# Performance work log

Hardware: AMD Instinct MI355X
Metric: run time of the kernel (lower is better)

The kernel has to match this reference:

```python
import jax, jax.numpy as jnp
import numpy as np

B, C, H, W, L = 8, 512, 32, 32, 10
CQK = C // 8
EPS = 1e-5


def conv1x1(x, Wt, b):
    # 1x1 conv == per-pixel linear: [O,C] x [B,C,H,W] -> [B,O,H,W]
    return jnp.einsum('oc,bchw->bohw', Wt, x) + b[None, :, None, None]


def batchnorm_train(x, g, b):
    # BatchNorm2d in training mode: batch stats over (N,H,W), biased variance
    m = x.mean(axis=(0, 2, 3))
    v = x.var(axis=(0, 2, 3))
    inv = jax.lax.rsqrt(v + EPS)
    return (x - m[None, :, None, None]) * (g * inv)[None, :, None, None] + b[None, :, None, None]


def setup_inputs() -> dict:
    key = jax.random.key(0)
    ks = jax.random.split(key, 24)
    s = lambda n: 1.0 / np.sqrt(n)
    inp = {
        'x': jax.random.normal(ks[0], (B, C, H, W), jnp.float32),
        'y': jax.random.normal(ks[1], (B, C, H, W), jnp.float32),
        'x_hidden': jax.random.normal(ks[2], (L, B, C, H, W), jnp.float32),
        'y_hidden': jax.random.normal(ks[3], (L, B, C, H, W), jnp.float32),
        'qW': jax.random.normal(ks[4], (CQK, C), jnp.float32) * s(C),
        'qb': jnp.zeros((CQK,), jnp.float32),
        'kW': jax.random.normal(ks[5], (CQK, C), jnp.float32) * s(C),
        'kb': jnp.zeros((CQK,), jnp.float32),
        'v1W': jax.random.normal(ks[6], (C, C), jnp.float32) * s(C),
        'v1b': jnp.zeros((C,), jnp.float32),
        'v2W': jax.random.normal(ks[7], (C, C), jnp.float32) * s(C),
        'v2b': jnp.zeros((C,), jnp.float32),
        'hw1': jnp.ones((L,), jnp.float32),
        'hw2': jnp.ones((L,), jnp.float32),
        'g1W1': jax.random.normal(ks[8], (64, C), jnp.float32) * s(C),
        'g1b1': jnp.zeros((64,), jnp.float32),
        'g1W2': jax.random.normal(ks[9], (1, 64), jnp.float32) * s(64),
        'g1b2': jnp.zeros((1,), jnp.float32),
        'g2W1': jax.random.normal(ks[10], (64, C), jnp.float32) * s(C),
        'g2b1': jnp.zeros((64,), jnp.float32),
        'g2W2': jax.random.normal(ks[11], (1, 64), jnp.float32) * s(64),
        'g2b2': jnp.zeros((1,), jnp.float32),
        'rW1': jax.random.normal(ks[12], (C, C), jnp.float32) * s(C),
        'rb1': jnp.zeros((C,), jnp.float32),
        'bn1g': jnp.ones((C,), jnp.float32),
        'bn1b': jnp.zeros((C,), jnp.float32),
        'rW2': jax.random.normal(ks[13], (C, C), jnp.float32) * s(C),
        'rb2': jnp.zeros((C,), jnp.float32),
        'bn2g': jnp.ones((C,), jnp.float32),
        'bn2b': jnp.zeros((C,), jnp.float32),
    }
    return inp


def reference(x, y, x_hidden, y_hidden, qW, qb, kW, kb, v1W, v1b, v2W, v2b,
              hw1, hw2, g1W1, g1b1, g1W2, g1b2, g2W1, g2b1, g2W2, g2b2,
              rW1, rb1, bn1g, bn1b, rW2, rb2, bn2g, bn2b):
    b_, c_, h_, w_ = x.shape
    n = h_ * w_

    def residual(z):
        z1 = jax.nn.relu(batchnorm_train(conv1x1(z, rW1, rb1), bn1g, bn1b))
        return batchnorm_train(conv1x1(z1, rW2, rb2), bn2g, bn2b)

    # QKV projections (1x1 convs), flattened to tokens
    q = conv1x1(x, qW, qb).reshape(b_, CQK, n).transpose(0, 2, 1)   # [B,N,Cqk]
    k = conv1x1(y, kW, kb).reshape(b_, CQK, n)                       # [B,Cqk,N]
    v1 = conv1x1(x, v1W, v1b).reshape(b_, c_, n)                     # [B,C,N]
    v2 = conv1x1(y, v2W, v2b).reshape(b_, c_, n)

    attn = jax.nn.softmax(jnp.einsum('bnd,bdm->bnm', q, k), axis=-1)  # [B,N,N]
    out1 = jnp.einsum('bcn,bmn->bcm', v1, attn).reshape(b_, c_, h_, w_)  # v1 @ attn^T
    out2 = jnp.einsum('bcn,bnm->bcm', v2, attn).reshape(b_, c_, h_, w_)  # v2 @ attn

    # hidden-layer weighted channel means -> gamma scalars
    num_layers = min(x_hidden.shape[0], L)
    xw = jax.nn.softmax(hw1[:num_layers])
    yw = jax.nn.softmax(hw2[:num_layers])
    x_hw = jnp.einsum('l,lbc->bc', xw, x_hidden[:num_layers].mean(axis=(3, 4)))  # [B,C]
    y_hw = jnp.einsum('l,lbc->bc', yw, y_hidden[:num_layers].mean(axis=(3, 4)))

    def gamma_gen(v, W1, b1, W2, b2):
        h1 = jax.nn.relu(v @ W1.T + b1)
        return (h1 @ W2.T + b2).reshape(b_, 1, 1, 1)

    gamma1 = gamma_gen(x_hw, g1W1, g1b1, g1W2, g1b2)
    gamma2 = gamma_gen(y_hw, g2W1, g2b1, g2W2, g2b2)

    out1 = jax.nn.relu(residual(gamma1 * out1) + x)
    out2 = jax.nn.relu(residual(gamma2 * out2) + y)
    return out1, out2
```

## Files before the change

kernel.cpp:

```cpp
#include <hip/hip_runtime.h>

#define BB 8
#define CC 512
#define NT 1024
#define LL 10
#define DQK 64
#define BN_EPS 1e-5f

using u16 = unsigned short;
typedef __attribute__((ext_vector_type(8))) short short8;
typedef __attribute__((ext_vector_type(4))) float f32x4;
typedef __attribute__((ext_vector_type(4))) float nf4;

__device__ __forceinline__ float waveSum(float v) {
#pragma unroll
  for (int o = 32; o; o >>= 1) v += __shfl_down(v, o, 64);
  return v;
}
__device__ __forceinline__ float waveMax(float v) {
#pragma unroll
  for (int o = 32; o; o >>= 1) v = fmaxf(v, __shfl_down(v, o, 64));
  return v;
}
__device__ __forceinline__ u16 f2bf(float f) {
  unsigned u = __float_as_uint(f);
  u += 0x7FFFu + ((u >> 16) & 1u);
  return (u16)(u >> 16);
}
__device__ __forceinline__ float bf2f(u16 h) {
  return __uint_as_float(((unsigned)h) << 16);
}
__device__ __forceinline__ void g2l16(const u16* g, void* l) {
  __builtin_amdgcn_global_load_lds(
      (const __attribute__((address_space(1))) unsigned int*)g,
      (__attribute__((address_space(3))) unsigned int*)l, 16, 0, 0);
}

struct PreArgs {
  const float *xh, *yh;
  float* lm;
  const float *v1W, *v2W, *rW1, *rW2;
  u16* Wdst;
  const float *qW, *kW;
  u16 *qh, *ql, *kh, *kl;
  const float *qb, *kb, *v1b, *v2b;
  float *qkb, *vb;
  const float *x, *y;
  u16 *xth, *xtl, *yth, *ytl;
};
__global__ __launch_bounds__(256) void pre_kernel(PreArgs a) {
  __shared__ float t[64][65];
  const int blk = blockIdx.x;
  if (blk < 20480) {
    int wid = blk * 4 + (threadIdx.x >> 6);
    int lane = threadIdx.x & 63;
    const int LBC = LL * BB * CC;
    const float* src = a.xh;
    int r = wid;
    if (wid >= LBC) { src = a.yh; r = wid - LBC; }
    const nf4* p = (const nf4*)(src + (size_t)r * NT);
    nf4 v0 = __builtin_nontemporal_load(p + lane);
    nf4 v1 = __builtin_nontemporal_load(p + 64 + lane);
    nf4 v2 = __builtin_nontemporal_load(p + 128 + lane);
    nf4 v3 = __builtin_nontemporal_load(p + 192 + lane);
    float s = ((v0.x + v0.y) + (v0.z + v0.w)) + ((v1.x + v1.y) + (v1.z + v1.w)) +
              ((v2.x + v2.y) + (v2.z + v2.w)) + ((v3.x + v3.y) + (v3.z + v3.w));
    s = waveSum(s);
    if (lane == 0) a.lm[wid] = s * (1.0f / NT);
  } else if (blk < 21504) {
    int rel = blk - 20480;
    const float* srcs[4] = {a.v1W, a.v2W, a.rW1, a.rW2};
    const float4* s4 = (const float4*)srcs[rel >> 8];
    int r = rel & 255;
    float4 v = s4[(size_t)r * 256 + threadIdx.x];
    uint2 o;
    o.x = (unsigned)f2bf(v.x) | ((unsigned)f2bf(v.y) << 16);
    o.y = (unsigned)f2bf(v.z) | ((unsigned)f2bf(v.w) << 16);
    ((uint2*)a.Wdst)[(size_t)rel * 256 + threadIdx.x] = o;
  } else if (blk < 21568) {
    int rel = blk - 21504;
    if (rel == 0) {
      int tt = threadIdx.x;
      if (tt < 64) a.qkb[tt] = a.qb[tt];
      else if (tt < 128) a.qkb[tt] = a.kb[tt - 64];
      a.vb[tt] = a.v1b[tt]; a.vb[tt + 256] = a.v1b[tt + 256];
      a.vb[tt + 512] = a.v2b[tt]; a.vb[tt + 768] = a.v2b[tt + 256];
    }
    const float* src = (rel < 32) ? a.qW : a.kW;
    u16* dh = (rel < 32) ? a.qh : a.kh;
    u16* dl = (rel < 32) ? a.ql : a.kl;
    int r = rel & 31;
    float4 v = ((const float4*)src)[(size_t)r * 256 + threadIdx.x];
    u16 h0 = f2bf(v.x), h1 = f2bf(v.y), h2 = f2bf(v.z), h3 = f2bf(v.w);
    u16 l0 = f2bf(v.x - bf2f(h0)), l1 = f2bf(v.y - bf2f(h1));
    u16 l2 = f2bf(v.z - bf2f(h2)), l3 = f2bf(v.w - bf2f(h3));
    uint2 oh, ol;
    oh.x = (unsigned)h0 | ((unsigned)h1 << 16); oh.y = (unsigned)h2 | ((unsigned)h3 << 16);
    ol.x = (unsigned)l0 | ((unsigned)l1 << 16); ol.y = (unsigned)l2 | ((unsigned)l3 << 16);
    ((uint2*)dh)[(size_t)r * 256 + threadIdx.x] = oh;
    ((uint2*)dl)[(size_t)r * 256 + threadIdx.x] = ol;
  } else {
    int rel = blk - 21568;
    int z = rel >> 7;
    const float* src = (z < 8) ? a.x : a.y;
    u16* dh = (z < 8) ? a.xth : a.yth;
    u16* dl = (z < 8) ? a.xtl : a.ytl;
    int b = z & 7;
    int n0 = (rel & 15) * 64, c0 = ((rel >> 4) & 7) * 64;
    int tc = threadIdx.x & 63, tr = threadIdx.x >> 6;
    const float* S = src + ((size_t)b * CC + c0) * NT + n0;
#pragma unroll
    for (int r = 0; r < 16; r++) {
      int c = tr + r * 4;
      t[c][tc] = S[(size_t)c * NT + tc];
    }
    __syncthreads();
    size_t base = ((size_t)b * NT + n0) * CC + c0;
#pragma unroll
    for (int r = 0; r < 16; r++) {
      int n = tr + r * 4;
      float v = t[tc][n];
      u16 h = f2bf(v);
      dh[base + (size_t)n * CC + tc] = h;
      dl[base + (size_t)n * CC + tc] = f2bf(v - bf2f(h));
    }
  }
}

__global__ __launch_bounds__(256) void gamma_kernel(
    const float* __restrict__ lm,
    const float* __restrict__ hw1, const float* __restrict__ hw2,
    const float* __restrict__ g1W1, const float* __restrict__ g1b1,
    const float* __restrict__ g1W2, const float* __restrict__ g1b2,
    const float* __restrict__ g2W1, const float* __restrict__ g2b1,
    const float* __restrict__ g2W2, const float* __restrict__ g2b2,
    float* __restrict__ gamma) {
  int which = blockIdx.x >> 3;
  int b = blockIdx.x & 7;
  const float* hw = which ? hw2 : hw1;
  const float* W1 = which ? g2W1 : g1W1;
  const float* b1 = which ? g2b1 : g1b1;
  const float* W2 = which ? g2W2 : g1W2;
  const float* b2 = which ? g2b2 : g1b2;
  __shared__ float sxhw[CC];
  __shared__ float wsm[LL];
  if (threadIdx.x == 0) {
    float mx = -1e30f;
    for (int l = 0; l < LL; l++) mx = fmaxf(mx, hw[l]);
    float den = 0.f, e[LL];
    for (int l = 0; l < LL; l++) { e[l] = __expf(hw[l] - mx); den += e[l]; }
    for (int l = 0; l < LL; l++) wsm[l] = e[l] / den;
  }
  __syncthreads();
  const float* lmb = lm + (size_t)which * LL * BB * CC + b * CC;
  for (int c = threadIdx.x; c < CC; c += blockDim.x) {
    float a = 0.f;
    for (int l = 0; l < LL; l++) a += wsm[l] * lmb[l * BB * CC + c];
    sxhw[c] = a;
  }
  __syncthreads();
  float contrib = 0.f;
  if (threadIdx.x < 64) {
    int d = threadIdx.x;
    float a = b1[d];
    const float* wr = W1 + d * CC;
    for (int c = 0; c < CC; c++) a = fmaf(wr[c], sxhw[c], a);
    contrib = W2[d] * fmaxf(a, 0.f);
  }
  contrib = waveSum(contrib);
  if (threadIdx.x == 0) gamma[which * BB + b] = contrib + b2[0];
}

__global__ __launch_bounds__(256) void transpose_attn_kernel(
    const u16* __restrict__ attn, u16* __restrict__ attnT) {
  __shared__ u16 t[64][66];
  int b = blockIdx.z;
  int n0 = blockIdx.y * 64, m0 = blockIdx.x * 64;
  int tc = threadIdx.x & 63, tr = threadIdx.x >> 6;
  const u16* S = attn + ((size_t)b * NT + n0) * NT + m0;
#pragma unroll
  for (int r = 0; r < 16; r++) {
    int nr = tr + r * 4;
    t[nr][tc] = S[(size_t)nr * NT + tc];
  }
  __syncthreads();
  u16* D = attnT + ((size_t)b * NT + m0) * NT + n0;
#pragma unroll
  for (int r = 0; r < 16; r++) {
    int mr = tr + r * 4;
    D[(size_t)mr * NT + tc] = t[tc][mr];
  }
}

template <int BN, int SMODE>
__global__ __launch_bounds__(256) void gemm_bf16(
    const u16* __restrict__ A, long long sA, int lda,
    const u16* __restrict__ B, long long sB, long long sB2, int ldb,
    void* __restrict__ C, long long sC, int ldc,
    int K, int storef32,
    const float* __restrict__ bias_row, int brs,
    const float* __restrict__ scale,
    float* __restrict__ pS, float* __restrict__ pS2) {
  constexpr int BM = 128, BK = 32;
  constexpr int WN = (BN == 128) ? 2 : 1;
  constexpr int WM = 4 / WN;
  constexpr int FM = BM / (WM * 16);
  constexpr int FN = BN / (WN * 16);
  __shared__ u16 As[BM * BK];
  __shared__ u16 Bs[BN * BK];
  const int bz = blockIdx.z;
  const int i0 = blockIdx.y * BM;
  const int j0 = blockIdx.x * BN;
  const u16* Ab = A + (size_t)bz * sA + (size_t)i0 * lda;
  const u16* Bb = B + (size_t)(bz & 7) * sB + (size_t)(bz >> 3) * sB2 + (size_t)j0 * ldb;
  const int tid = threadIdx.x;
  const int lane = tid & 63;
  const int wave = tid >> 6;
  const int wr = wave / WN, wc = wave % WN;
  const int fr = lane & 15;
  const int kg = lane >> 4;
  const int arow = tid >> 2;
  const int aq = tid & 3;

  f32x4 acc[FM][FN] = {};

  for (int k0 = 0; k0 < K; k0 += BK) {
#pragma unroll
    for (int c = 0; c < (BM * BK * 2) / 4096; c++)
      g2l16(Ab + (size_t)(arow + c * 64) * lda + k0 + aq * 8,
            (char*)As + c * 4096 + tid * 16);
#pragma unroll
    for (int c = 0; c < (BN * BK * 2) / 4096; c++)
      g2l16(Bb + (size_t)(arow + c * 64) * ldb + k0 + aq * 8,
            (char*)Bs + c * 4096 + tid * 16);
    __syncthreads();
    short8 fa[FM], fb[FN];
#pragma unroll
    for (int i = 0; i < FM; i++)
      fa[i] = *(const short8*)&As[(wr * FM * 16 + i * 16 + fr) * BK + kg * 8];
#pragma unroll
    for (int j = 0; j < FN; j++)
      fb[j] = *(const short8*)&Bs[(wc * FN * 16 + j * 16 + fr) * BK + kg * 8];
#pragma unroll
    for (int i = 0; i < FM; i++)
#pragma unroll
      for (int j = 0; j < FN; j++)
        acc[i][j] = __builtin_amdgcn_mfma_f32_16x16x32_bf16(fa[i], fb[j], acc[i][j], 0, 0, 0);
    __syncthreads();
  }

  const float scl = scale ? scale[bz] : 1.0f;
  const float* brow = bias_row ? bias_row + (size_t)bz * brs : nullptr;
  float* Cf = (float*)C + (size_t)bz * sC;
  u16* Ch = (u16*)C + (size_t)bz * sC;
  float cs[FN] = {}, cs2[FN] = {};
  float rs[FM * 4] = {}, rs2[FM * 4] = {};
#pragma unroll
  for (int i = 0; i < FM; i++) {
#pragma unroll
    for (int j = 0; j < FN; j++) {
      int col = j0 + wc * FN * 16 + j * 16 + fr;
#pragma unroll
      for (int r = 0; r < 4; r++) {
        int row = i0 + wr * FM * 16 + i * 16 + kg * 4 + r;
        float rb = brow ? brow[row] : 0.0f;
        float v = (acc[i][j][r] + rb) * scl;
        if constexpr (SMODE == 1) { cs[j] += v; cs2[j] += v * v; }
        if constexpr (SMODE == 2) { rs[i * 4 + r] += v; rs2[i * 4 + r] += v * v; }
        if (storef32) Cf[(size_t)row * ldc + col] = v;
        else Ch[(size_t)row * ldc + col] = f2bf(v);
      }
    }
  }

  if constexpr (SMODE == 1) {
    __shared__ float sred[2][4][FN][16];
#pragma unroll
    for (int j = 0; j < FN; j++) {
      float s = cs[j], s2 = cs2[j];
      s += __shfl_xor(s, 16, 64); s += __shfl_xor(s, 32, 64);
      s2 += __shfl_xor(s2, 16, 64); s2 += __shfl_xor(s2, 32, 64);
      if (lane < 16) { sred[0][wr][j][lane] = s; sred[1][wr][j][lane] = s2; }
    }
    __syncthreads();
    if (tid < FN * 16) {
      int j = tid >> 4, f = tid & 15;
      float s = sred[0][0][j][f] + sred[0][1][j][f] + sred[0][2][j][f] + sred[0][3][j][f];
      float s2 = sred[1][0][j][f] + sred[1][1][j][f] + sred[1][2][j][f] + sred[1][3][j][f];
      int col = j0 + j * 16 + f;
      int chain = (int)(blockIdx.y >> 6), ib = (int)(blockIdx.y & 63);
      pS[((size_t)chain * 512 + col) * 64 + ib] = s;
      pS2[((size_t)chain * 512 + col) * 64 + ib] = s2;
    }
  }
  if constexpr (SMODE == 2) {
#pragma unroll
    for (int i = 0; i < FM; i++)
#pragma unroll
      for (int r = 0; r < 4; r++) {
        float s = rs[i * 4 + r], s2 = rs2[i * 4 + r];
        s += __shfl_xor(s, 1, 64); s += __shfl_xor(s, 2, 64);
        s += __shfl_xor(s, 4, 64); s += __shfl_xor(s, 8, 64);
        s2 += __shfl_xor(s2, 1, 64); s2 += __shfl_xor(s2, 2, 64);
        s2 += __shfl_xor(s2, 4, 64); s2 += __shfl_xor(s2, 8, 64);
        if (fr == 0) {
          int row = i0 + wr * FM * 16 + i * 16 + kg * 4 + r;
          pS[((size_t)bz * 512 + row) * 128 + blockIdx.x] = s;
          pS2[((size_t)bz * 512 + row) * 128 + blockIdx.x] = s2;
        }
      }
  }
}

__global__ __launch_bounds__(256) void gemm_split(
    const u16* __restrict__ Ah_, const u16* __restrict__ Al_, long long sA, int lda,
    const u16* __restrict__ Bh_, const u16* __restrict__ Bl_, long long sB, int ldb,
    float* __restrict__ Cf, u16* __restrict__ Ch, u16* __restrict__ Cl,
    long long sC, int ldc, int K, const float* __restrict__ bias_col, int bcs) {
  constexpr int BM = 128, BN = 64, BK = 32;
  constexpr int FM = 2, FN = 4;
  __shared__ u16 Ahs[BM * BK];
  __shared__ u16 Als[BM * BK];
  __shared__ u16 Bhs[BN * BK];
  __shared__ u16 Bls[BN * BK];
  const int bz = blockIdx.z;
  const int i0 = blockIdx.y * BM;
  const int j0 = blockIdx.x * BN;
  const u16* Abh = Ah_ + (size_t)bz * sA + (size_t)i0 * lda;
  const u16* Abl = Al_ + (size_t)bz * sA + (size_t)i0 * lda;
  const u16* Bbh = Bh_ + (size_t)bz * sB + (size_t)j0 * ldb;
  const u16* Bbl = Bl_ + (size_t)bz * sB + (size_t)j0 * ldb;
  const int tid = threadIdx.x;
  const int lane = tid & 63;
  const int wr = tid >> 6;
  const int fr = lane & 15;
  const int kg = lane >> 4;
  const int arow = tid >> 2;
  const int aq = tid & 3;

  f32x4 acc[FM][FN] = {};

  for (int k0 = 0; k0 < K; k0 += BK) {
#pragma unroll
    for (int c = 0; c < 2; c++) {
      g2l16(Abh + (size_t)(arow + c * 64) * lda + k0 + aq * 8,
            (char*)Ahs + c * 4096 + tid * 16);
      g2l16(Abl + (size_t)(arow + c * 64) * lda + k0 + aq * 8,
            (char*)Als + c * 4096 + tid * 16);
    }
    g2l16(Bbh + (size_t)arow * ldb + k0 + aq * 8, (char*)Bhs + tid * 16);
    g2l16(Bbl + (size_t)arow * ldb + k0 + aq * 8, (char*)Bls + tid * 16);
    __syncthreads();
    short8 fah[FM], fal[FM], fbh[FN], fbl[FN];
#pragma unroll
    for (int i = 0; i < FM; i++) {
      fah[i] = *(const short8*)&Ahs[(wr * 32 + i * 16 + fr) * BK + kg * 8];
      fal[i] = *(const short8*)&Als[(wr * 32 + i * 16 + fr) * BK + kg * 8];
    }
#pragma unroll
    for (int j = 0; j < FN; j++) {
      fbh[j] = *(const short8*)&Bhs[(j * 16 + fr) * BK + kg * 8];
      fbl[j] = *(const short8*)&Bls[(j * 16 + fr) * BK + kg * 8];
    }
#pragma unroll
    for (int i = 0; i < FM; i++)
#pragma unroll
      for (int j = 0; j < FN; j++) {
        acc[i][j] = __builtin_amdgcn_mfma_f32_16x16x32_bf16(fah[i], fbh[j], acc[i][j], 0, 0, 0);
        acc[i][j] = __builtin_amdgcn_mfma_f32_16x16x32_bf16(fah[i], fbl[j], acc[i][j], 0, 0, 0);
        acc[i][j] = __builtin_amdgcn_mfma_f32_16x16x32_bf16(fal[i], fbh[j], acc[i][j], 0, 0, 0);
      }
    __syncthreads();
  }

  const float* bcol = bias_col ? bias_col + (size_t)bz * bcs : nullptr;
  float* Cfb = Cf ? Cf + (size_t)bz * sC : nullptr;
  u16* Chb = Ch ? Ch + (size_t)bz * sC : nullptr;
  u16* Clb = Cl ? Cl + (size_t)bz * sC : nullptr;
#pragma unroll
  for (int i = 0; i < FM; i++) {
#pragma unroll
    for (int j = 0; j < FN; j++) {
      int col = j0 + j * 16 + fr;
      float cb = bcol ? bcol[col] : 0.0f;
#pragma unroll
      for (int r = 0; r < 4; r++) {
        int row = i0 + wr * 32 + i * 16 + kg * 4 + r;
        float v = acc[i][j][r] + cb;
        if (Cfb) {
          Cfb[(size_t)row * ldc + col] = v;
        } else {
          u16 h = f2bf(v);
          Chb[(size_t)row * ldc + col] = h;
          Clb[(size_t)row * ldc + col] = f2bf(v - bf2f(h));
        }
      }
    }
  }
}

__global__ __launch_bounds__(256) void softmax_bf_kernel(
    const float* __restrict__ S, u16* __restrict__ A) {
  const float4* row = (const float4*)(S + (size_t)blockIdx.x * NT);
  float4 v = row[threadIdx.x];
  __shared__ float sb[4];
  __shared__ float broad;
  int lane = threadIdx.x & 63, wid = threadIdx.x >> 6;
  float mx = fmaxf(fmaxf(v.x, v.y), fmaxf(v.z, v.w));
  mx = waveMax(mx);
  if (lane == 0) sb[wid] = mx;
  __syncthreads();
  if (threadIdx.x == 0) broad = fmaxf(fmaxf(sb[0], sb[1]), fmaxf(sb[2], sb[3]));
  __syncthreads();
  mx = broad;
  v.x = __expf(v.x - mx); v.y = __expf(v.y - mx);
  v.z = __expf(v.z - mx); v.w = __expf(v.w - mx);
  float s = v.x + v.y + v.z + v.w;
  s = waveSum(s);
  __syncthreads();
  if (lane == 0) sb[wid] = s;
  __syncthreads();
  if (threadIdx.x == 0) broad = sb[0] + sb[1] + sb[2] + sb[3];
  __syncthreads();
  float inv = 1.0f / broad;
  uint2 o;
  o.x = (unsigned)f2bf(v.x * inv) | ((unsigned)f2bf(v.y * inv) << 16);
  o.y = (unsigned)f2bf(v.z * inv) | ((unsigned)f2bf(v.w * inv) << 16);
  ((uint2*)(A + (size_t)blockIdx.x * NT))[threadIdx.x] = o;
}

template <int NP>
__global__ __launch_bounds__(128) void bnstats_reduce_np(
    const float* __restrict__ pS, const float* __restrict__ pS2,
    const float* __restrict__ g, const float* __restrict__ bet,
    float* __restrict__ scale, float* __restrict__ shift) {
  int cg = blockIdx.x;
  int c = cg & 511;
  int t = threadIdx.x;
  float s = 0.f, s2 = 0.f;
  if (t < NP) { s = pS[(size_t)cg * NP + t]; s2 = pS2[(size_t)cg * NP + t]; }
  s = waveSum(s); s2 = waveSum(s2);
  __shared__ float sb[4];
  int lane = t & 63, wid = t >> 6;
  if (lane == 0) { sb[wid] = s; sb[wid + 2] = s2; }
  __syncthreads();
  if (t == 0) {
    float S = sb[0] + sb[1];
    float S2 = sb[2] + sb[3];
    const float invn = 1.0f / (BB * NT);
    float mean = S * invn;
    float var = S2 * invn - mean * mean;
    float inv = rsqrtf(var + BN_EPS);
    float sc = g[c] * inv;
    scale[cg] = sc;
    shift[cg] = bet[c] - mean * sc;
  }
}

__global__ __launch_bounds__(256) void bn_apply_kernel(
    const u16* __restrict__ Z, u16* __restrict__ Zo,
    const float* __restrict__ scale, const float* __restrict__ shift) {
  size_t e4 = (size_t)blockIdx.x * 256 + threadIdx.x;
  int chain = (int)(e4 >> 20);
  int c = (int)(e4 & 127) * 4 + chain * 512;
  uint2 u = ((const uint2*)Z)[e4];
  float a = bf2f((u16)u.x), b = bf2f((u16)(u.x >> 16));
  float d = bf2f((u16)u.y), e = bf2f((u16)(u.y >> 16));
  a = fmaxf(fmaf(a, scale[c], shift[c]), 0.f);
  b = fmaxf(fmaf(b, scale[c + 1], shift[c + 1]), 0.f);
  d = fmaxf(fmaf(d, scale[c + 2], shift[c + 2]), 0.f);
  e = fmaxf(fmaf(e, scale[c + 3], shift[c + 3]), 0.f);
  uint2 o;
  o.x = (unsigned)f2bf(a) | ((unsigned)f2bf(b) << 16);
  o.y = (unsigned)f2bf(d) | ((unsigned)f2bf(e) << 16);
  ((uint2*)Zo)[e4] = o;
}

__global__ __launch_bounds__(256) void bn_final_kernel(
    const u16* __restrict__ Z2, const float* __restrict__ X, const float* __restrict__ Y,
    const float* __restrict__ scale, const float* __restrict__ shift,
    float* __restrict__ Out) {
  size_t e = (size_t)blockIdx.x * 256 + threadIdx.x;
  int chain = (int)(e >> 20);
  size_t ec = e & 1048575;
  int c = (int)(ec >> 11);
  int r = (int)(ec & 2047);
  int b = r >> 8;
  uint2 u = ((const uint2*)Z2)[e];
  float a0 = bf2f((u16)u.x), a1 = bf2f((u16)(u.x >> 16));
  float a2 = bf2f((u16)u.y), a3 = bf2f((u16)(u.y >> 16));
  float sc = scale[c + chain * 512], sh = shift[c + chain * 512];
  size_t xi = ((size_t)b * CC + c) * 256 + (r & 255);
  const float* Xs = chain ? Y : X;
  float4 xv = ((const float4*)Xs)[xi];
  float4 o;
  o.x = fmaxf(fmaf(a0, sc, sh) + xv.x, 0.f);
  o.y = fmaxf(fmaf(a1, sc, sh) + xv.y, 0.f);
  o.z = fmaxf(fmaf(a2, sc, sh) + xv.z, 0.f);
  o.w = fmaxf(fmaf(a3, sc, sh) + xv.w, 0.f);
  ((float4*)(Out + (size_t)chain * 4194304))[xi] = o;
}

extern "C" void kernel_launch(void* const* d_in, const int* in_sizes, int n_in,
                              void* d_out, int out_size, void* d_ws, size_t ws_size,
                              hipStream_t stream) {
  (void)in_sizes; (void)n_in; (void)out_size; (void)ws_size;
  const float* x    = (const float*)d_in[0];
  const float* y    = (const float*)d_in[1];
  const float* xh   = (const float*)d_in[2];
  const float* yh   = (const float*)d_in[3];
  const float* qW   = (const float*)d_in[4];
  const float* qb   = (const float*)d_in[5];
  const float* kW   = (const float*)d_in[6];
  const float* kb   = (const float*)d_in[7];
  const float* v1W  = (const float*)d_in[8];
  const float* v1b  = (const float*)d_in[9];
  const float* v2W  = (const float*)d_in[10];
  const float* v2b  = (const float*)d_in[11];
  const float* hw1  = (const float*)d_in[12];
  const float* hw2  = (const float*)d_in[13];
  const float* g1W1 = (const float*)d_in[14];
  const float* g1b1 = (const float*)d_in[15];
  const float* g1W2 = (const float*)d_in[16];
  const float* g1b2 = (const float*)d_in[17];
  const float* g2W1 = (const float*)d_in[18];
  const float* g2b1 = (const float*)d_in[19];
  const float* g2W2 = (const float*)d_in[20];
  const float* g2b2 = (const float*)d_in[21];
  const float* rW1  = (const float*)d_in[22];
  const float* bn1g = (const float*)d_in[24];
  const float* bn1b = (const float*)d_in[25];
  const float* rW2  = (const float*)d_in[26];
  const float* bn2g = (const float*)d_in[28];
  const float* bn2b = (const float*)d_in[29];
  float* out = (float*)d_out;

  float* ws  = (float*)d_ws;
  float* lm  = ws;
  float* gam = ws + 81920;
  float* scA = ws + 81936;
  float* shA = ws + 82960;
  float* qkb = ws + 83984;
  float* vb  = ws + 84112;
  float* pS  = ws + 85136;
  float* pS2 = ws + 347280;
  float* S   = ws + 609424;
  u16* U     = (u16*)(ws + 8998032);
  u16* Wqh = U;
  u16* Wql = U + 32768;
  u16* Wkh = U + 65536;
  u16* Wkl = U + 98304;
  u16* Wv1 = U + 131072;
  u16* Wv2 = U + 393216;
  u16* Wr1 = U + 655360;
  u16* Wr2 = U + 917504;
  u16* xth = U + 1179648;
  u16* yth = xth + 4194304;
  u16* xtl = yth + 4194304;
  u16* ytl = xtl + 4194304;
  u16* q_h = ytl + 4194304;
  u16* q_l = q_h + 524288;
  u16* k_h = q_l + 524288;
  u16* k_l = k_h + 524288;
  u16* v1  = k_l + 524288;
  u16* v2  = v1 + 4194304;
  u16* attn  = v2 + 4194304;
  u16* attnT = attn + 8388608;
  u16* o1t = xth;
  u16* z0  = v1;
  u16* z1  = xth;
  u16* z2  = attn;

  PreArgs pa;
  pa.xh = xh; pa.yh = yh; pa.lm = lm;
  pa.v1W = v1W; pa.v2W = v2W; pa.rW1 = rW1; pa.rW2 = rW2; pa.Wdst = Wv1;
  pa.qW = qW; pa.kW = kW; pa.qh = Wqh; pa.ql = Wql; pa.kh = Wkh; pa.kl = Wkl;
  pa.qb = qb; pa.kb = kb; pa.v1b = v1b; pa.v2b = v2b; pa.qkb = qkb; pa.vb = vb;
  pa.x = x; pa.y = y; pa.xth = xth; pa.xtl = xtl; pa.yth = yth; pa.ytl = ytl;
  pre_kernel<<<23616, 256, 0, stream>>>(pa);
  gamma_kernel<<<16, 256, 0, stream>>>(lm, hw1, hw2, g1W1, g1b1, g1W2, g1b2,
                                       g2W1, g2b1, g2W2, g2b2, gam);

  gemm_bf16<64, 0><<<dim3(128, 4, 2), 256, 0, stream>>>(
      Wv1, 262144, CC, xth, 4194304, 0, CC, v1, 4194304, BB * NT, CC, 0, vb, 512,
      nullptr, nullptr, nullptr);
  gemm_split<<<dim3(1, 64, 2), 256, 0, stream>>>(
      xth, xtl, 4194304, CC, Wqh, Wql, 65536, CC,
      nullptr, q_h, q_l, 1048576, DQK, CC, qkb, 64);

  gemm_split<<<dim3(16, 8, 8), 256, 0, stream>>>(
      q_h, q_l, (long long)NT * DQK, DQK, k_h, k_l, (long long)NT * DQK, DQK,
      S, nullptr, nullptr, (long long)NT * NT, NT, DQK, nullptr, 0);
  softmax_bf_kernel<<<BB * NT, 256, 0, stream>>>(S, attn);
  transpose_attn_kernel<<<dim3(16, 16, 8), 256, 0, stream>>>(attn, attnT);

  gemm_bf16<64, 0><<<dim3(8, 8, 16), 256, 0, stream>>>(
      attn, (long long)NT * NT, NT, v1, NT, 4194304, BB * NT,
      o1t, (long long)NT * CC, CC, NT, 0, nullptr, 0, gam, nullptr, nullptr);

  gemm_bf16<64, 1><<<dim3(8, 128, 1), 256, 0, stream>>>(
      o1t, 0, CC, Wr1, 0, 0, CC, z0, 0, CC, CC, 0, nullptr, 0, nullptr, pS, pS2);
  bnstats_reduce_np<64><<<1024, 128, 0, stream>>>(pS, pS2, bn1g, bn1b, scA, shA);
  bn_apply_kernel<<<8192, 256, 0, stream>>>(z0, z1, scA, shA);
  gemm_bf16<64, 2><<<dim3(128, 4, 2), 256, 0, stream>>>(
      Wr2, 0, CC, z1, 4194304, 0, CC, z2, 4194304, BB * NT, CC, 0, nullptr, 0, nullptr,
      pS, pS2);
  bnstats_reduce_np<128><<<1024, 128, 0, stream>>>(pS, pS2, bn2g, bn2b, scA, shA);
  bn_final_kernel<<<8192, 256, 0, stream>>>(z2, x, y, scA, shA, out);
}
```

Baseline: 278.9 us.

## Spread hidden-mean reduction blocks across GEMM launches and defer gamma scaling

New measurement: 268.5 us. 3.8% less time.

```diff
diff --git a/kernel.cpp b/kernel.cpp
--- a/kernel.cpp
+++ b/kernel.cpp
@@ -36,9 +36,27 @@
       (__attribute__((address_space(3))) unsigned int*)l, 16, 0, 0);
 }
 
+__device__ __forceinline__ void hidden_mean_block(
+    int mb, const float* __restrict__ xh, const float* __restrict__ yh,
+    float* __restrict__ lm) {
+  int wid = mb * 4 + ((int)threadIdx.x >> 6);
+  int lane = threadIdx.x & 63;
+  const int LBC = LL * BB * CC;
+  const float* src = xh;
+  int r = wid;
+  if (wid >= LBC) { src = yh; r = wid - LBC; }
+  const nf4* p = (const nf4*)(src + (size_t)r * NT);
+  nf4 v0 = __builtin_nontemporal_load(p + lane);
+  nf4 v1 = __builtin_nontemporal_load(p + 64 + lane);
+  nf4 v2 = __builtin_nontemporal_load(p + 128 + lane);
+  nf4 v3 = __builtin_nontemporal_load(p + 192 + lane);
+  float s = ((v0.x + v0.y) + (v0.z + v0.w)) + ((v1.x + v1.y) + (v1.z + v1.w)) +
+            ((v2.x + v2.y) + (v2.z + v2.w)) + ((v3.x + v3.y) + (v3.z + v3.w));
+  s = waveSum(s);
+  if (lane == 0) lm[wid] = s * (1.0f / NT);
+}
+
 struct PreArgs {
-  const float *xh, *yh;
-  float* lm;
   const float *v1W, *v2W, *rW1, *rW2;
   u16* Wdst;
   const float *qW, *kW;
@@ -51,24 +69,8 @@
 __global__ __launch_bounds__(256) void pre_kernel(PreArgs a) {
   __shared__ float t[64][65];
   const int blk = blockIdx.x;
-  if (blk < 20480) {
-    int wid = blk * 4 + (threadIdx.x >> 6);
-    int lane = threadIdx.x & 63;
-    const int LBC = LL * BB * CC;
-    const float* src = a.xh;
-    int r = wid;
-    if (wid >= LBC) { src = a.yh; r = wid - LBC; }
-    const nf4* p = (const nf4*)(src + (size_t)r * NT);
-    nf4 v0 = __builtin_nontemporal_load(p + lane);
-    nf4 v1 = __builtin_nontemporal_load(p + 64 + lane);
-    nf4 v2 = __builtin_nontemporal_load(p + 128 + lane);
-    nf4 v3 = __builtin_nontemporal_load(p + 192 + lane);
-    float s = ((v0.x + v0.y) + (v0.z + v0.w)) + ((v1.x + v1.y) + (v1.z + v1.w)) +
-              ((v2.x + v2.y) + (v2.z + v2.w)) + ((v3.x + v3.y) + (v3.z + v3.w));
-    s = waveSum(s);
-    if (lane == 0) a.lm[wid] = s * (1.0f / NT);
-  } else if (blk < 21504) {
-    int rel = blk - 20480;
+  if (blk < 1024) {
+    int rel = blk;
     const float* srcs[4] = {a.v1W, a.v2W, a.rW1, a.rW2};
     const float4* s4 = (const float4*)srcs[rel >> 8];
     int r = rel & 255;
@@ -77,8 +79,8 @@
     o.x = (unsigned)f2bf(v.x) | ((unsigned)f2bf(v.y) << 16);
     o.y = (unsigned)f2bf(v.z) | ((unsigned)f2bf(v.w) << 16);
     ((uint2*)a.Wdst)[(size_t)rel * 256 + threadIdx.x] = o;
-  } else if (blk < 21568) {
-    int rel = blk - 21504;
+  } else if (blk < 1088) {
+    int rel = blk - 1024;
     if (rel == 0) {
       int tt = threadIdx.x;
       if (tt < 64) a.qkb[tt] = a.qb[tt];
@@ -100,7 +102,7 @@
     ((uint2*)dh)[(size_t)r * 256 + threadIdx.x] = oh;
     ((uint2*)dl)[(size_t)r * 256 + threadIdx.x] = ol;
   } else {
-    int rel = blk - 21568;
+    int rel = blk - 1088;
     int z = rel >> 7;
     const float* src = (z < 8) ? a.x : a.y;
     u16* dh = (z < 8) ? a.xth : a.yth;
@@ -192,7 +194,7 @@
   }
 }
 
-template <int BN, int SMODE>
+template <int BN, int SMODE, int GMODE>
 __global__ __launch_bounds__(256) void gemm_bf16(
     const u16* __restrict__ A, long long sA, int lda,
     const u16* __restrict__ B, long long sB, long long sB2, int ldb,
@@ -200,7 +202,10 @@
     int K, int storef32,
     const float* __restrict__ bias_row, int brs,
     const float* __restrict__ scale,
-    float* __restrict__ pS, float* __restrict__ pS2) {
+    float* __restrict__ pS, float* __restrict__ pS2,
+    int xbits, int ybits, int nReal,
+    int meanBase, const float* __restrict__ xh, const float* __restrict__ yh,
+    float* __restrict__ lm) {
   constexpr int BM = 128, BK = 32;
   constexpr int WN = (BN == 128) ? 2 : 1;
   constexpr int WM = 4 / WN;
@@ -208,9 +213,18 @@
   constexpr int FN = BN / (WN * 16);
   __shared__ u16 As[BM * BK];
   __shared__ u16 Bs[BN * BK];
-  const int bz = blockIdx.z;
-  const int i0 = blockIdx.y * BM;
-  const int j0 = blockIdx.x * BN;
+  int bx, by, bz;
+  if (nReal > 0) {
+    int id = blockIdx.x;
+    if (id >= nReal) { hidden_mean_block(meanBase + (id - nReal), xh, yh, lm); return; }
+    bx = id & ((1 << xbits) - 1);
+    by = (id >> xbits) & ((1 << ybits) - 1);
+    bz = id >> (xbits + ybits);
+  } else {
+    bx = blockIdx.x; by = blockIdx.y; bz = blockIdx.z;
+  }
+  const int i0 = by * BM;
+  const int j0 = bx * BN;
   const u16* Ab = A + (size_t)bz * sA + (size_t)i0 * lda;
   const u16* Bb = B + (size_t)(bz & 7) * sB + (size_t)(bz >> 3) * sB2 + (size_t)j0 * ldb;
   const int tid = threadIdx.x;
@@ -249,7 +263,7 @@
     __syncthreads();
   }
 
-  const float scl = scale ? scale[bz] : 1.0f;
+  const float scl = (GMODE == 0 && scale) ? scale[bz] : 1.0f;
   const float* brow = bias_row ? bias_row + (size_t)bz * brs : nullptr;
   float* Cf = (float*)C + (size_t)bz * sC;
   u16* Ch = (u16*)C + (size_t)bz * sC;
@@ -264,7 +278,9 @@
       for (int r = 0; r < 4; r++) {
         int row = i0 + wr * FM * 16 + i * 16 + kg * 4 + r;
         float rb = brow ? brow[row] : 0.0f;
-        float v = (acc[i][j][r] + rb) * scl;
+        float sc2 = scl;
+        if constexpr (GMODE == 1) sc2 = scale[((row >> 13) << 3) + ((row >> 10) & 7)];
+        float v = (acc[i][j][r] + rb) * sc2;
         if constexpr (SMODE == 1) { cs[j] += v; cs2[j] += v * v; }
         if constexpr (SMODE == 2) { rs[i * 4 + r] += v; rs2[i * 4 + r] += v * v; }
         if (storef32) Cf[(size_t)row * ldc + col] = v;
@@ -288,7 +304,7 @@
       float s = sred[0][0][j][f] + sred[0][1][j][f] + sred[0][2][j][f] + sred[0][3][j][f];
       float s2 = sred[1][0][j][f] + sred[1][1][j][f] + sred[1][2][j][f] + sred[1][3][j][f];
       int col = j0 + j * 16 + f;
-      int chain = (int)(blockIdx.y >> 6), ib = (int)(blockIdx.y & 63);
+      int chain = by >> 6, ib = by & 63;
       pS[((size_t)chain * 512 + col) * 64 + ib] = s;
       pS2[((size_t)chain * 512 + col) * 64 + ib] = s2;
     }
@@ -305,8 +321,8 @@
         s2 += __shfl_xor(s2, 4, 64); s2 += __shfl_xor(s2, 8, 64);
         if (fr == 0) {
           int row = i0 + wr * FM * 16 + i * 16 + kg * 4 + r;
-          pS[((size_t)bz * 512 + row) * 128 + blockIdx.x] = s;
-          pS2[((size_t)bz * 512 + row) * 128 + blockIdx.x] = s2;
+          pS[((size_t)bz * 512 + row) * 128 + bx] = s;
+          pS2[((size_t)bz * 512 + row) * 128 + bx] = s2;
         }
       }
   }
@@ -316,16 +332,26 @@
     const u16* __restrict__ Ah_, const u16* __restrict__ Al_, long long sA, int lda,
     const u16* __restrict__ Bh_, const u16* __restrict__ Bl_, long long sB, int ldb,
     float* __restrict__ Cf, u16* __restrict__ Ch, u16* __restrict__ Cl,
-    long long sC, int ldc, int K, const float* __restrict__ bias_col, int bcs) {
+    long long sC, int ldc, int K, const float* __restrict__ bias_col, int bcs,
+    int xbits, int ybits, int nReal,
+    int meanBase, const float* __restrict__ xh, const float* __restrict__ yh,
+    float* __restrict__ lm) {
   constexpr int BM = 128, BN = 64, BK = 32;
   constexpr int FM = 2, FN = 4;
   __shared__ u16 Ahs[BM * BK];
   __shared__ u16 Als[BM * BK];
   __shared__ u16 Bhs[BN * BK];
   __shared__ u16 Bls[BN * BK];
-  const int bz = blockIdx.z;
-  const int i0 = blockIdx.y * BM;
-  const int j0 = blockIdx.x * BN;
+  int bx, by, bz;
+  {
+    int id = blockIdx.x;
+    if (id >= nReal) { hidden_mean_block(meanBase + (id - nReal), xh, yh, lm); return; }
+    bx = id & ((1 << xbits) - 1);
+    by = (id >> xbits) & ((1 << ybits) - 1);
+    bz = id >> (xbits + ybits);
+  }
+  const int i0 = by * BM;
+  const int j0 = bx * BN;
   const u16* Abh = Ah_ + (size_t)bz * sA + (size_t)i0 * lda;
   const u16* Abl = Al_ + (size_t)bz * sA + (size_t)i0 * lda;
   const u16* Bbh = Bh_ + (size_t)bz * sB + (size_t)j0 * ldb;
@@ -572,39 +598,42 @@
   u16* z2  = attn;
 
   PreArgs pa;
-  pa.xh = xh; pa.yh = yh; pa.lm = lm;
   pa.v1W = v1W; pa.v2W = v2W; pa.rW1 = rW1; pa.rW2 = rW2; pa.Wdst = Wv1;
   pa.qW = qW; pa.kW = kW; pa.qh = Wqh; pa.ql = Wql; pa.kh = Wkh; pa.kl = Wkl;
   pa.qb = qb; pa.kb = kb; pa.v1b = v1b; pa.v2b = v2b; pa.qkb = qkb; pa.vb = vb;
   pa.x = x; pa.y = y; pa.xth = xth; pa.xtl = xtl; pa.yth = yth; pa.ytl = ytl;
-  pre_kernel<<<23616, 256, 0, stream>>>(pa);
+  pre_kernel<<<3136, 256, 0, stream>>>(pa);
+
+  gemm_bf16<128, 0, 0><<<512 + 5120, 256, 0, stream>>>(
+      Wv1, 262144, CC, xth, 4194304, 0, CC, v1, 4194304, BB * NT, CC, 0, vb, 512,
+      nullptr, nullptr, nullptr, 6, 2, 512, 0, xh, yh, lm);
+  gemm_split<<<128 + 3072, 256, 0, stream>>>(
+      xth, xtl, 4194304, CC, Wqh, Wql, 65536, CC,
+      nullptr, q_h, q_l, 1048576, DQK, CC, qkb, 64,
+      0, 6, 128, 5120, xh, yh, lm);
+
+  gemm_split<<<1024 + 4096, 256, 0, stream>>>(
+      q_h, q_l, (long long)NT * DQK, DQK, k_h, k_l, (long long)NT * DQK, DQK,
+      S, nullptr, nullptr, (long long)NT * NT, NT, DQK, nullptr, 0,
+      4, 3, 1024, 8192, xh, yh, lm);
+  softmax_bf_kernel<<<BB * NT, 256, 0, stream>>>(S, attn);
+  transpose_attn_kernel<<<dim3(16, 16, 8), 256, 0, stream>>>(attn, attnT);
+
+  gemm_bf16<128, 0, 0><<<512 + 8192, 256, 0, stream>>>(
+      attn, (long long)NT * NT, NT, v1, NT, 4194304, BB * NT,
+      o1t, (long long)NT * CC, CC, NT, 0, nullptr, 0, nullptr, nullptr, nullptr,
+      2, 3, 512, 12288, xh, yh, lm);
+
   gamma_kernel<<<16, 256, 0, stream>>>(lm, hw1, hw2, g1W1, g1b1, g1W2, g1b2,
                                        g2W1, g2b1, g2W2, g2b2, gam);
-
-  gemm_bf16<64, 0><<<dim3(128, 4, 2), 256, 0, stream>>>(
-      Wv1, 262144, CC, xth, 4194304, 0, CC, v1, 4194304, BB * NT, CC, 0, vb, 512,
-      nullptr, nullptr, nullptr);
-  gemm_split<<<dim3(1, 64, 2), 256, 0, stream>>>(
-      xth, xtl, 4194304, CC, Wqh, Wql, 65536, CC,
-      nullptr, q_h, q_l, 1048576, DQK, CC, qkb, 64);
-
-  gemm_split<<<dim3(16, 8, 8), 256, 0, stream>>>(
-      q_h, q_l, (long long)NT * DQK, DQK, k_h, k_l, (long long)NT * DQK, DQK,
-      S, nullptr, nullptr, (long long)NT * NT, NT, DQK, nullptr, 0);
-  softmax_bf_kernel<<<BB * NT, 256, 0, stream>>>(S, attn);
-  transpose_attn_kernel<<<dim3(16, 16, 8), 256, 0, stream>>>(attn, attnT);
-
-  gemm_bf16<64, 0><<<dim3(8, 8, 16), 256, 0, stream>>>(
-      attn, (long long)NT * NT, NT, v1, NT, 4194304, BB * NT,
-      o1t, (long long)NT * CC, CC, NT, 0, nullptr, 0, gam, nullptr, nullptr);
-
-  gemm_bf16<64, 1><<<dim3(8, 128, 1), 256, 0, stream>>>(
-      o1t, 0, CC, Wr1, 0, 0, CC, z0, 0, CC, CC, 0, nullptr, 0, nullptr, pS, pS2);
+  gemm_bf16<64, 1, 1><<<dim3(8, 128, 1), 256, 0, stream>>>(
+      o1t, 0, CC, Wr1, 0, 0, CC, z0, 0, CC, CC, 0, nullptr, 0, gam, pS, pS2,
+      0, 0, 0, 0, nullptr, nullptr, nullptr);
   bnstats_reduce_np<64><<<1024, 128, 0, stream>>>(pS, pS2, bn1g, bn1b, scA, shA);
   bn_apply_kernel<<<8192, 256, 0, stream>>>(z0, z1, scA, shA);
-  gemm_bf16<64, 2><<<dim3(128, 4, 2), 256, 0, stream>>>(
+  gemm_bf16<64, 2, 0><<<dim3(128, 4, 2), 256, 0, stream>>>(
       Wr2, 0, CC, z1, 4194304, 0, CC, z2, 4194304, BB * NT, CC, 0, nullptr, 0, nullptr,
-      pS, pS2);
+      pS, pS2, 0, 0, 0, 0, nullptr, nullptr, nullptr);
   bnstats_reduce_np<128><<<1024, 128, 0, stream>>>(pS, pS2, bn2g, bn2b, scA, shA);
   bn_final_kernel<<<8192, 256, 0, stream>>>(z2, x, y, scA, shA, out);
 }
```
